# Kernel optimization log

Hardware: AMD Instinct MI355X
Metric: run time of the kernel (lower is better)

## Reference

```python
import jax, jax.numpy as jnp
import numpy as np

N, M, D = 32768, 4096, 32


def setup_inputs() -> dict:
    key = jax.random.key(0)
    k1, k2, k3 = jax.random.split(key, 3)
    X = jax.random.normal(k1, (N, D), dtype=jnp.float32)
    centers = jax.random.normal(k2, (M, D), dtype=jnp.float32)
    # fitted Nystrom coefficients (params from .fit); b = Vj(1) in the Genred formula
    alphas = jax.random.normal(k3, (M, 1), dtype=jnp.float32) * 0.05
    sigma = jnp.ones((1,), dtype=jnp.float32)  # Pm(1) kernel lengthscale g
    return {"X": X, "centers": centers, "alphas": alphas, "sigma": sigma}


def reference(X, centers, alphas, sigma):
    # Genred formula: Exp(SqDist(x/g, y/g) * IntInv(-2)) * b, reduced over j (axis=1)
    g = sigma[0]
    xs = X / g           # [N, D]
    ys = centers / g     # [M, D]
    x2 = jnp.sum(xs * xs, axis=1, keepdims=True)            # [N, 1]
    y2 = jnp.sum(ys * ys, axis=1, keepdims=True).T          # [1, M]
    sqdist = x2 + y2 - 2.0 * (xs @ ys.T)                    # [N, M]
    k = jnp.exp(-0.5 * sqdist)                              # RBF kernel values
    return k @ alphas                                       # [N, 1]
```

## Files before the change

### kernel.cpp

```cpp
#include <hip/hip_runtime.h>

#define NN 32768
#define MM 4096
#define DD 32

typedef short short8 __attribute__((ext_vector_type(8)));
typedef float f32x4 __attribute__((ext_vector_type(4)));

#define ROWTILES 4
#define WAVES 4

__device__ __forceinline__ unsigned short f2bf(float f) {
    unsigned u = __float_as_uint(f);
    unsigned r = 0x7FFFu + ((u >> 16) & 1u);
    return (unsigned short)((u + r) >> 16);
}
__device__ __forceinline__ float bf2f(unsigned short h) {
    return __uint_as_float(((unsigned)h) << 16);
}

__global__ __launch_bounds__(256) void prep_kern(
    const float* __restrict__ X, const float* __restrict__ C,
    const float* __restrict__ alphas, const float* __restrict__ sigma,
    unsigned short* __restrict__ Xh, unsigned short* __restrict__ Xl,
    unsigned short* __restrict__ Ch, unsigned short* __restrict__ Cl,
    float* __restrict__ Bx, float* __restrict__ w)
{
    const int i = blockIdx.x * 256 + threadIdx.x;
    const int row = i >> 2;
    const int q = i & 3;
    const float g = sigma[0];
    const float LA = 1.44269504088896340736f / (g * g);

    const bool isX = (row < NN);
    const int crow = isX ? row : (row - NN);
    const float* src = (isX ? X + (size_t)row * DD : C + (size_t)crow * DD) + q * 8;
    unsigned short* dh = (isX ? Xh + (size_t)row * DD : Ch + (size_t)crow * DD) + q * 8;
    unsigned short* dl = (isX ? Xl + (size_t)row * DD : Cl + (size_t)crow * DD) + q * 8;
    const float scale = isX ? LA : 1.0f;

    float4 a = ((const float4*)src)[0];
    float4 b = ((const float4*)src)[1];
    float vv[8] = {a.x, a.y, a.z, a.w, b.x, b.y, b.z, b.w};
    float s2 = 0.f;
    short8 hv, lv;
#pragma unroll
    for (int e = 0; e < 8; ++e) {
        float v = vv[e];
        s2 = fmaf(v, v, s2);
        float sv = v * scale;
        unsigned short h = f2bf(sv);
        hv[e] = (short)h;
        lv[e] = (short)f2bf(sv - bf2f(h));
    }
    *(short8*)dh = hv;
    *(short8*)dl = lv;

    s2 += __shfl_xor(s2, 1, 64);
    s2 += __shfl_xor(s2, 2, 64);
    if (q == 0) {
        float bb = -0.5f * LA * s2;
        if (isX) Bx[row] = bb;
        else     w[crow] = alphas[crow] * exp2f(bb);
    }
}

template <int MS>
__global__ __launch_bounds__(256, 4) void rbf_mfma_lds(
    const unsigned short* __restrict__ Xh, const unsigned short* __restrict__ Xl,
    const unsigned short* __restrict__ Ch, const unsigned short* __restrict__ Cl,
    const float* __restrict__ Bx, const float* __restrict__ w,
    float* __restrict__ part)
{
    constexpr int MPER = MM / MS;
    constexpr int NT = MPER / 16;
    __shared__ unsigned short sCh[MPER * DD];
    __shared__ unsigned short sCl[MPER * DD];
    __shared__ float sw[MPER];

    const int tid = threadIdx.x;
    const int wave = tid >> 6;
    const int lane = tid & 63;
    const int l15 = lane & 15;
    const int lhi = lane >> 4;
    const int rowbase = (blockIdx.x * WAVES + wave) * (16 * ROWTILES);
    const int slice = blockIdx.y;
    const int j0 = slice * MPER;

    const char* lh = (const char*)sCh;
    const char* ll = (const char*)sCl;

    {
        const float4* gh = (const float4*)(Ch + (size_t)j0 * DD);
        const float4* gl = (const float4*)(Cl + (size_t)j0 * DD);
        constexpr int NV = MPER * DD / 8;
        for (int o = tid; o < NV; o += 256) {
            ((float4*)sCh)[o] = gh[o];
            ((float4*)sCl)[o] = gl[o];
        }
        if (tid < MPER) sw[tid] = w[j0 + tid];
    }

    short8 ah[ROWTILES], al[ROWTILES];
#pragma unroll
    for (int t = 0; t < ROWTILES; ++t) {
        int r = rowbase + t * 16 + l15;
        ah[t] = *(const short8*)(Xh + (size_t)r * DD + lhi * 8);
        al[t] = *(const short8*)(Xl + (size_t)r * DD + lhi * 8);
    }

    f32x4 acc[ROWTILES];
#pragma unroll
    for (int t = 0; t < ROWTILES; ++t) acc[t] = (f32x4){0.f, 0.f, 0.f, 0.f};

    __syncthreads();

    const int lbase = l15 * 64 + lhi * 16;
    const f32x4 kZero = {0.f, 0.f, 0.f, 0.f};

#pragma unroll 2
    for (int jt = 0; jt < NT; ++jt) {
        short8 bh = *(const short8*)(lh + lbase + jt * 1024);
        short8 bl = *(const short8*)(ll + lbase + jt * 1024);
        float wj = sw[jt * 16 + l15];
#pragma unroll
        for (int t = 0; t < ROWTILES; ++t) {
            f32x4 d;
            d = __builtin_amdgcn_mfma_f32_16x16x32_bf16(ah[t], bl, kZero, 0, 0, 0);
            d = __builtin_amdgcn_mfma_f32_16x16x32_bf16(al[t], bh, d, 0, 0, 0);
            d = __builtin_amdgcn_mfma_f32_16x16x32_bf16(ah[t], bh, d, 0, 0, 0);
#pragma unroll
            for (int rr = 0; rr < 4; ++rr)
                acc[t][rr] = fmaf(wj, __builtin_amdgcn_exp2f(d[rr]), acc[t][rr]);
        }
    }

#pragma unroll
    for (int t = 0; t < ROWTILES; ++t)
#pragma unroll
        for (int rr = 0; rr < 4; ++rr) {
            float v = acc[t][rr];
            v += __shfl_xor(v, 1, 64);
            v += __shfl_xor(v, 2, 64);
            v += __shfl_xor(v, 4, 64);
            v += __shfl_xor(v, 8, 64);
            acc[t][rr] = v;
        }
    if (l15 == 0) {
#pragma unroll
        for (int t = 0; t < ROWTILES; ++t) {
            float4 bxv = *(const float4*)&Bx[rowbase + t * 16 + lhi * 4];
            f32x4 o;
            o[0] = acc[t][0] * __builtin_amdgcn_exp2f(bxv.x);
            o[1] = acc[t][1] * __builtin_amdgcn_exp2f(bxv.y);
            o[2] = acc[t][2] * __builtin_amdgcn_exp2f(bxv.z);
            o[3] = acc[t][3] * __builtin_amdgcn_exp2f(bxv.w);
            *(f32x4*)&part[(size_t)slice * NN + rowbase + t * 16 + lhi * 4] = o;
        }
    }
}

template <int MS>
__global__ __launch_bounds__(256) void reduce_kern(const float* __restrict__ part,
                                                   float* __restrict__ out) {
    int i = blockIdx.x * 256 + threadIdx.x;
    float s = 0.f;
#pragma unroll
    for (int k = 0; k < MS; ++k) s += part[(size_t)k * NN + i];
    out[i] = s;
}

__global__ __launch_bounds__(256) void wkern(const float* __restrict__ C,
                                             const float* __restrict__ alphas,
                                             const float* __restrict__ sigma,
                                             float* __restrict__ w) {
    int j = blockIdx.x * 256 + threadIdx.x;
    if (j >= MM) return;
    float g = sigma[0];
    float inv_g2 = 1.0f / (g * g);
    const float4* cp = (const float4*)(C + (size_t)j * DD);
    float y2 = 0.f;
#pragma unroll
    for (int q = 0; q < DD / 4; ++q) {
        float4 v = cp[q];
        y2 = fmaf(v.x, v.x, y2);
        y2 = fmaf(v.y, v.y, y2);
        y2 = fmaf(v.z, v.z, y2);
        y2 = fmaf(v.w, v.w, y2);
    }
    w[j] = alphas[j] * exp2f(-0.5f * inv_g2 * 1.44269504088896340736f * y2);
}

__global__ __launch_bounds__(128) void rbf_valu(const float* __restrict__ X,
                                                const float* __restrict__ C,
                                                const float* __restrict__ w,
                                                const float* __restrict__ sigma,
                                                float* __restrict__ out) {
    const int row = blockIdx.x * 128 + threadIdx.x;
    const float g = sigma[0];
    const float A = 1.44269504088896340736f / (g * g);
    float x[DD];
    const float4* xp = (const float4*)(X + (size_t)row * DD);
#pragma unroll
    for (int q = 0; q < DD / 4; ++q) {
        float4 v = xp[q];
        x[4 * q + 0] = v.x; x[4 * q + 1] = v.y;
        x[4 * q + 2] = v.z; x[4 * q + 3] = v.w;
    }
    float x2 = 0.f;
#pragma unroll
    for (int d = 0; d < DD; ++d) x2 = fmaf(x[d], x[d], x2);
    const float B = -0.5f * A * x2;
    float acc = 0.f;
#pragma unroll 2
    for (int j = 0; j < MM; ++j) {
        const float* cj = C + (size_t)j * DD;
        float d0 = 0.f, d1 = 0.f, d2 = 0.f, d3 = 0.f;
#pragma unroll
        for (int d = 0; d < DD; d += 4) {
            d0 = fmaf(cj[d + 0], x[d + 0], d0);
            d1 = fmaf(cj[d + 1], x[d + 1], d1);
            d2 = fmaf(cj[d + 2], x[d + 2], d2);
            d3 = fmaf(cj[d + 3], x[d + 3], d3);
        }
        float dot = (d0 + d1) + (d2 + d3);
        acc = fmaf(w[j], exp2f(fmaf(dot, A, B)), acc);
    }
    out[row] = acc;
}

extern "C" void kernel_launch(void* const* d_in, const int* in_sizes, int n_in,
                              void* d_out, int out_size, void* d_ws, size_t ws_size,
                              hipStream_t stream) {
    const float* X  = (const float*)d_in[0];
    const float* C  = (const float*)d_in[1];
    const float* al = (const float*)d_in[2];
    const float* sg = (const float*)d_in[3];
    float* out = (float*)d_out;

    size_t off = 0;
    unsigned short* Xh = (unsigned short*)((char*)d_ws + off); off += (size_t)NN * DD * 2;
    unsigned short* Xl = (unsigned short*)((char*)d_ws + off); off += (size_t)NN * DD * 2;
    unsigned short* Ch = (unsigned short*)((char*)d_ws + off); off += (size_t)MM * DD * 2;
    unsigned short* Cl = (unsigned short*)((char*)d_ws + off); off += (size_t)MM * DD * 2;
    float* Bx = (float*)((char*)d_ws + off); off += (size_t)NN * 4;
    float* w  = (float*)((char*)d_ws + off); off += (size_t)MM * 4;
    float* part = (float*)((char*)d_ws + off);
    const size_t base = off;

    const size_t need32 = base + (size_t)32 * NN * 4;
    const size_t need8  = base + (size_t)8 * NN * 4;

    if (ws_size >= need8) {
        prep_kern<<<(NN + MM) * 4 / 256, 256, 0, stream>>>(X, C, al, sg, Xh, Xl, Ch, Cl, Bx, w);
        if (ws_size >= need32) {
            dim3 grid(NN / (WAVES * 16 * ROWTILES), 32);
            rbf_mfma_lds<32><<<grid, 64 * WAVES, 0, stream>>>(Xh, Xl, Ch, Cl, Bx, w, part);
            reduce_kern<32><<<NN / 256, 256, 0, stream>>>(part, out);
        } else {
            dim3 grid(NN / (WAVES * 16 * ROWTILES), 8);
            rbf_mfma_lds<8><<<grid, 64 * WAVES, 0, stream>>>(Xh, Xl, Ch, Cl, Bx, w, part);
            reduce_kern<8><<<NN / 256, 256, 0, stream>>>(part, out);
        }
    } else {
        float* wf = (float*)d_ws;
        wkern<<<MM / 256, 256, 0, stream>>>(C, al, sg, wf);
        rbf_valu<<<NN / 128, 128, 0, stream>>>(X, C, wf, sg, out);
    }
}
```

Baseline: 40.08 us.

## Software-pipeline MFMA and exp epilogue across alternating center tiles

Restructures the inner loop into a two-stage A/B pipeline: the MFMAs for the next 16-center tile are issued while the exp2/FMA epilogue of the previous tile runs, and LDS reads are prefetched one step ahead. This is meant to hide MFMA latency behind VALU transcendental work. The extra live registers are paid for by lowering the launch-bounds occupancy hint from 4 to 3 blocks per CU. The loop is also fully unrolled, which can grow code size.

New measurement: 42.26 us. 1.05x slower.

```diff
diff --git a/kernel.cpp b/kernel.cpp
--- a/kernel.cpp
+++ b/kernel.cpp
@@ -66,7 +66,7 @@
 }
 
 template <int MS>
-__global__ __launch_bounds__(256, 4) void rbf_mfma_lds(
+__global__ __launch_bounds__(256, 3) void rbf_mfma_lds(
     const unsigned short* __restrict__ Xh, const unsigned short* __restrict__ Xl,
     const unsigned short* __restrict__ Ch, const unsigned short* __restrict__ Cl,
     const float* __restrict__ Bx, const float* __restrict__ w,
@@ -74,6 +74,7 @@
 {
     constexpr int MPER = MM / MS;
     constexpr int NT = MPER / 16;
+    static_assert((NT & 1) == 0, "NT must be even for the A/B pipeline");
     __shared__ unsigned short sCh[MPER * DD];
     __shared__ unsigned short sCl[MPER * DD];
     __shared__ float sw[MPER];
@@ -118,22 +119,57 @@
     const int lbase = l15 * 64 + lhi * 16;
     const f32x4 kZero = {0.f, 0.f, 0.f, 0.f};
 
-#pragma unroll 2
-    for (int jt = 0; jt < NT; ++jt) {
-        short8 bh = *(const short8*)(lh + lbase + jt * 1024);
-        short8 bl = *(const short8*)(ll + lbase + jt * 1024);
-        float wj = sw[jt * 16 + l15];
-#pragma unroll
-        for (int t = 0; t < ROWTILES; ++t) {
-            f32x4 d;
-            d = __builtin_amdgcn_mfma_f32_16x16x32_bf16(ah[t], bl, kZero, 0, 0, 0);
-            d = __builtin_amdgcn_mfma_f32_16x16x32_bf16(al[t], bh, d, 0, 0, 0);
-            d = __builtin_amdgcn_mfma_f32_16x16x32_bf16(ah[t], bh, d, 0, 0, 0);
-#pragma unroll
-            for (int rr = 0; rr < 4; ++rr)
-                acc[t][rr] = fmaf(wj, __builtin_amdgcn_exp2f(d[rr]), acc[t][rr]);
-        }
-    }
+#define READB(k, BH, BL, WJ)                                   \
+    do {                                                        \
+        BH = *(const short8*)(lh + lbase + (k) * 1024);         \
+        BL = *(const short8*)(ll + lbase + (k) * 1024);         \
+        WJ = sw[(k) * 16 + l15];                                \
+    } while (0)
+
+#define MFMAJT(BH, BL, D)                                                        \
+    do {                                                                          \
+        _Pragma("unroll")                                                         \
+        for (int t = 0; t < ROWTILES; ++t) {                                      \
+            f32x4 dd;                                                             \
+            dd = __builtin_amdgcn_mfma_f32_16x16x32_bf16(ah[t], BL, kZero, 0, 0, 0); \
+            dd = __builtin_amdgcn_mfma_f32_16x16x32_bf16(al[t], BH, dd, 0, 0, 0); \
+            dd = __builtin_amdgcn_mfma_f32_16x16x32_bf16(ah[t], BH, dd, 0, 0, 0); \
+            D[t] = dd;                                                            \
+        }                                                                         \
+    } while (0)
+
+#define EPILOG(D, WJ)                                                             \
+    do {                                                                          \
+        _Pragma("unroll")                                                         \
+        for (int t = 0; t < ROWTILES; ++t)                                        \
+            _Pragma("unroll")                                                     \
+            for (int rr = 0; rr < 4; ++rr)                                        \
+                acc[t][rr] = fmaf(WJ, __builtin_amdgcn_exp2f(D[t][rr]), acc[t][rr]); \
+    } while (0)
+
+    short8 bAh, bAl, bBh, bBl;
+    float wA, wB;
+    f32x4 dA[ROWTILES], dB[ROWTILES];
+
+    READB(0, bAh, bAl, wA);
+    READB(1, bBh, bBl, wB);
+    MFMAJT(bAh, bAl, dA);
+
+#pragma unroll
+    for (int k = 0; k < NT; k += 2) {
+        float wAn = wA, wBn = wB;
+        if (k + 2 < NT) READB(k + 2, bAh, bAl, wAn);
+        MFMAJT(bBh, bBl, dB);
+        EPILOG(dA, wA);
+        wA = wAn;
+        if (k + 3 < NT) READB(k + 3, bBh, bBl, wBn);
+        if (k + 2 < NT) MFMAJT(bAh, bAl, dA);
+        EPILOG(dB, wB);
+        wB = wBn;
+    }
+#undef READB
+#undef MFMAJT
+#undef EPILOG
 
 #pragma unroll
     for (int t = 0; t < ROWTILES; ++t)
```
